# Kernel optimization log

Measured on AMD Instinct MI355X. Metric: run time of the kernel, lower is better.

The kernel has to match this reference:

```python
import jax, jax.numpy as jnp
import numpy as np

LN_EPS = 1e-5


def _conv2d(x, w, b, pad):
    # x: [B,C,H,W], w: [O,I,k,k] (torch OIHW layout)
    out = jax.lax.conv_general_dilated(
        x, w, (1, 1), [(pad, pad), (pad, pad)],
        dimension_numbers=('NCHW', 'OIHW', 'NCHW'))
    return out + b[None, :, None, None]


def _deform_conv2d(x, offset, w, b, k, pad):
    # torchvision.ops.deform_conv2d, offset_groups=1, stride=1, dilation=1.
    # offset layout: [B, 2*k*k, H, W] with (dy, dx) interleaved per kernel tap.
    B, C, H, W = x.shape
    off = offset.reshape(B, k * k, 2, H, W)
    dy, dx = off[:, :, 0], off[:, :, 1]                      # [B,kk,H,W]
    ky, kx = jnp.meshgrid(jnp.arange(k, dtype=x.dtype),
                          jnp.arange(k, dtype=x.dtype), indexing='ij')
    py = (jnp.arange(H, dtype=x.dtype)[None, None, :, None]
          - pad + ky.reshape(-1)[None, :, None, None] + dy)   # sample rows
    px = (jnp.arange(W, dtype=x.dtype)[None, None, None, :]
          - pad + kx.reshape(-1)[None, :, None, None] + dx)   # sample cols
    y0 = jnp.floor(py)
    x0 = jnp.floor(px)
    fy = py - y0
    fx = px - x0
    xf = x.reshape(B, C, H * W)
    gather = jax.vmap(lambda xb, ib: xb[:, ib])               # [C,HW],[K]->[C,K]

    def corner(yc, xc, wt):
        valid = (yc >= 0) & (yc < H) & (xc >= 0) & (xc < W)
        idx = (jnp.clip(yc, 0, H - 1) * W
               + jnp.clip(xc, 0, W - 1)).astype(jnp.int32).reshape(B, -1)
        g = gather(xf, idx).reshape(B, C, k * k, H, W)
        return g * (wt * valid.astype(x.dtype))[:, None]

    # bilinear sample with zero padding outside the image
    acc = (corner(y0, x0, (1 - fy) * (1 - fx))
           + corner(y0, x0 + 1, (1 - fy) * fx)
           + corner(y0 + 1, x0, fy * (1 - fx))
           + corner(y0 + 1, x0 + 1, fy * fx))                 # [B,C,kk,H,W]
    out = jnp.einsum('bckhw,ock->bohw', acc, w.reshape(w.shape[0], C, k * k))
    return out + b[None, :, None, None]


def _deform_branch(xs, off_w, off_b, conv_w, conv_b, k, pad):
    # DeformableConv2d.forward: offset conv, deform_conv2d with conv's own
    # weight/bias, then the plain conv applied AGAIN on the result.
    offset = _conv2d(xs, off_w, off_b, pad)
    d = _deform_conv2d(xs, offset, conv_w, conv_b, k, pad)
    return _conv2d(d, conv_w, conv_b, pad)


def reference(x, H, W, fc1_w, fc1_b, off3_w, off3_b, conv3_w, conv3_b,
              off5_w, off5_b, conv5_w, conv5_b, ln_g, ln_b, fc2_w, fc2_b):
    B, N, _ = x.shape
    h = x @ fc1_w.T + fc1_b                                  # [B,N,hid]
    C = h.shape[-1]
    C2 = C // 2
    x1 = jnp.transpose(h[..., :C2], (0, 2, 1)).reshape(B, C2, H, W)
    x2 = jnp.transpose(h[..., C2:], (0, 2, 1)).reshape(B, C2, H, W)
    x1 = _deform_branch(x1, off3_w, off3_b, conv3_w, conv3_b, 3, 1)
    x2 = _deform_branch(x2, off5_w, off5_b, conv5_w, conv5_b, 5, 2)
    y = jnp.concatenate([x1, x2], axis=1)                    # [B,C,H,W]
    y = jnp.transpose(y.reshape(B, C, N), (0, 2, 1))         # [B,N,C]
    mu = jnp.mean(y, axis=-1, keepdims=True)
    var = jnp.mean(jnp.square(y - mu), axis=-1, keepdims=True)
    y = (y - mu) * jax.lax.rsqrt(var + LN_EPS) * ln_g + ln_b
    y = jax.nn.gelu(y, approximate=False)                    # nn.GELU default
    return y @ fc2_w.T + fc2_b


def setup_inputs() -> dict:
    key = jax.random.key(0)
    ks = jax.random.split(key, 16)
    B, H, W, Cin, Chid = 4, 32, 32, 256, 1024
    C2 = Chid // 2
    N = H * W
    r = lambda k, s, sc: jax.random.normal(k, s, dtype=jnp.float32) * sc
    return {
        'x': r(ks[0], (B, N, Cin), 1.0),
        'H': H, 'W': W,
        'fc1_w': r(ks[1], (Chid, Cin), 0.02),
        'fc1_b': r(ks[2], (Chid,), 0.02),
        'off3_w': r(ks[3], (2 * 9, C2, 3, 3), 0.01),
        'off3_b': r(ks[4], (2 * 9,), 0.01),
        'conv3_w': r(ks[5], (C2, C2, 3, 3), 0.02),
        'conv3_b': r(ks[6], (C2,), 0.02),
        'off5_w': r(ks[7], (2 * 25, C2, 5, 5), 0.01),
        'off5_b': r(ks[8], (2 * 25,), 0.01),
        'conv5_w': r(ks[9], (C2, C2, 5, 5), 0.02),
        'conv5_b': r(ks[10], (C2,), 0.02),
        'ln_g': jnp.ones((Chid,), jnp.float32),
        'ln_b': jnp.zeros((Chid,), jnp.float32),
        'fc2_w': r(ks[11], (Cin, Chid), 0.02),
        'fc2_b': r(ks[12], (Cin,), 0.02),
    }
```

## Files before the change

### kernel.cpp

```cpp
#include <hip/hip_runtime.h>

#define B_    4
#define H_    32
#define W_    32
#define N_    1024
#define CIN_  256
#define CHID_ 1024
#define C2_   512

typedef __attribute__((ext_vector_type(8))) short short8b;
typedef __attribute__((ext_vector_type(4))) float f32x4;

__device__ __forceinline__ unsigned int f2bf2(float lo, float hi) {
    unsigned int ul = __float_as_uint(lo);
    unsigned int uh = __float_as_uint(hi);
    ul += 0x7fffu + ((ul >> 16) & 1u);
    uh += 0x7fffu + ((uh >> 16) & 1u);
    return (ul >> 16) | (uh & 0xffff0000u);
}
__device__ __forceinline__ unsigned short f2bf(float f) {
    unsigned int u = __float_as_uint(f);
    u += 0x7fffu + ((u >> 16) & 1u);
    return (unsigned short)(u >> 16);
}
__device__ __forceinline__ unsigned int cvtpk(float lo, float hi) {
    unsigned int r;
    asm("v_cvt_pk_bf16_f32 %0, %1, %2" : "=v"(r) : "v"(lo), "v"(hi));
    return r;
}
__device__ __forceinline__ float bflo(unsigned int u) { return __uint_as_float(u << 16); }
__device__ __forceinline__ float bfhi(unsigned int u) { return __uint_as_float(u & 0xffff0000u); }

#define ROWP 40
#define MFMA_(a, b, c) __builtin_amdgcn_mfma_f32_16x16x32_bf16(a, b, c, 0, 0, 0)

template<int X> struct Log2 { static constexpr int v = 1 + Log2<X/2>::v; };
template<> struct Log2<1> { static constexpr int v = 0; };

struct ASet { uint4 r0, r1, r2, r3; float4 cw; };
struct BSet { short8b b0, b1, b2, b3; };

template<int AMODE, int KS, int CH, int OUTMODE, int GX, int IMGX = 0>
__global__ __launch_bounds__(512, 2)
void cgemm(const void* __restrict__ Asrc, int lda,
           const unsigned short* __restrict__ Bp, int nk32,
           int tcnt, int KK,
           const float* __restrict__ bias, void* __restrict__ Cout,
           int ldo, int O, int nO16,
           const short4* __restrict__ cidx, const float4* __restrict__ cwt)
{
    constexpr int CHS = Log2<CH>::v;
    __shared__ unsigned short As[2][2][64 * ROWP];

    const int tid = threadIdx.x;
    int m0, o0, tbeg, zslab;
    if constexpr (GX > 0) {
        const int bid = blockIdx.x;
        if constexpr (IMGX) {
            const int b8 = bid & 7, rest = bid >> 3;
            o0 = ((((b8 & 1) << 1) | (rest & 1))) * 128;
            m0 = (((b8 >> 1) << 4) | (rest >> 1)) * 64;
        } else {
            o0 = (bid & (GX - 1)) * 128;
            m0 = (bid / GX) * 64;
        }
        tbeg = 0; zslab = 0;
    } else {
        o0 = 0;
        m0 = blockIdx.y * 64;
        zslab = blockIdx.z;
        tbeg = zslab * tcnt;
    }

    const int srow = tid >> 3;
    const int sk8  = (tid & 7) << 3;
    const int am = m0 + srow;
    const int an = am & (N_ - 1), ab = am >> 10;
    const int ay = an >> 5, ax = an & 31;

    const int lane = tid & 63, wid = tid >> 6;
    const int wr = (wid >> 2) * 32, wc = (wid & 3) * 32;
    const int l15 = lane & 15, lk = (lane >> 4) * 8;

    const int o16a = min((o0 + wc) >> 4, nO16 - 1);
    const int o16b = min((o0 + wc + 16) >> 4, nO16 - 1);
    const unsigned short* bbA = Bp + (size_t)o16a * nk32 * 512 + lane * 8;
    const unsigned short* bbB = Bp + (size_t)o16b * nk32 * 512 + lane * 8;

    const int T = tcnt << CHS;
    const int qbase = (tbeg << CHS) * 2;

    const float* fp = nullptr;
    const unsigned short* sp = nullptr;
    bool svalid = false;
    const unsigned short *g0p = nullptr, *g1p = nullptr,
                         *g2p = nullptr, *g3p = nullptr;
    float4 curCw = {0.f, 0.f, 0.f, 0.f};
    short4 ciPref = {0, 0, 0, 0};
    float4 cwPref = {0.f, 0.f, 0.f, 0.f};

    if constexpr (AMODE == 0) {
        fp = (const float*)Asrc + (size_t)am * lda + sk8;
    } else if constexpr (AMODE == 2) {
        ciPref = cidx[(size_t)am * KK + tbeg];
        cwPref = cwt [(size_t)am * KK + tbeg];
    }

    auto advanceTap = [&](int tp) {
        if constexpr (AMODE == 1) {
            const int PAD = KS / 2;
            const int ty = tp / KS, tx = tp - ty * KS;
            const int yy = ay + ty - PAD, xx = ax + tx - PAD;
            svalid = (yy >= 0 && yy < H_ && xx >= 0 && xx < W_);
            if (svalid)
                sp = (const unsigned short*)Asrc
                   + (size_t)((ab << 10) | (yy << 5) | xx) * lda + sk8;
        } else if constexpr (AMODE == 2) {
            const unsigned short* base = (const unsigned short*)Asrc;
            g0p = base + (size_t)(int)ciPref.x * lda + sk8;
            g1p = base + (size_t)(int)ciPref.y * lda + sk8;
            g2p = base + (size_t)(int)ciPref.z * lda + sk8;
            g3p = base + (size_t)(int)ciPref.w * lda + sk8;
            curCw = cwPref;
            if (tp + 1 < tbeg + tcnt) {
                ciPref = cidx[(size_t)am * KK + tp + 1];
                cwPref = cwt [(size_t)am * KK + tp + 1];
            }
        }
    };

    auto loadRaw = [&](ASet& S, int u) {
        if constexpr (AMODE == 0) {
            S.r0 = *(const uint4*)(fp + (u << 6));
            S.r1 = *(const uint4*)(fp + (u << 6) + 4);
        } else if constexpr (AMODE == 1) {
            S.r0 = svalid ? *(const uint4*)(sp + (u << 6))
                          : make_uint4(0u, 0u, 0u, 0u);
        } else {
            S.r0 = *(const uint4*)(g0p + (u << 6));
            S.r1 = *(const uint4*)(g1p + (u << 6));
            S.r2 = *(const uint4*)(g2p + (u << 6));
            S.r3 = *(const uint4*)(g3p + (u << 6));
            S.cw = curCw;
        }
    };

    auto bl1 = [](unsigned a, unsigned b, unsigned c, unsigned d, float4 cw) {
        const float lo = cw.x * bflo(a) + cw.y * bflo(b)
                       + cw.z * bflo(c) + cw.w * bflo(d);
        const float hi = cw.x * bfhi(a) + cw.y * bfhi(b)
                       + cw.z * bfhi(c) + cw.w * bfhi(d);
        return cvtpk(lo, hi);
    };

    auto blendWrite = [&](ASet& S, int buf) {
        uint4 o;
        if constexpr (AMODE == 0) {
            o = make_uint4(cvtpk(__uint_as_float(S.r0.x), __uint_as_float(S.r0.y)),
                           cvtpk(__uint_as_float(S.r0.z), __uint_as_float(S.r0.w)),
                           cvtpk(__uint_as_float(S.r1.x), __uint_as_float(S.r1.y)),
                           cvtpk(__uint_as_float(S.r1.z), __uint_as_float(S.r1.w)));
        } else if constexpr (AMODE == 1) {
            o = S.r0;
        } else {
            o = make_uint4(bl1(S.r0.x, S.r1.x, S.r2.x, S.r3.x, S.cw),
                           bl1(S.r0.y, S.r1.y, S.r2.y, S.r3.y, S.cw),
                           bl1(S.r0.z, S.r1.z, S.r2.z, S.r3.z, S.cw),
                           bl1(S.r0.w, S.r1.w, S.r2.w, S.r3.w, S.cw));
        }
        *(uint4*)&As[buf][sk8 >> 5][srow * ROWP + (sk8 & 31)] = o;
    };

    auto loadB = [&](BSet& Bv, int g) {
        const int q = qbase + 2 * g;
        Bv.b0 = *(const short8b*)(bbA + (size_t)q * 512);
        Bv.b1 = *(const short8b*)(bbA + (size_t)(q + 1) * 512);
        Bv.b2 = *(const short8b*)(bbB + (size_t)q * 512);
        Bv.b3 = *(const short8b*)(bbB + (size_t)(q + 1) * 512);
    };

    f32x4 acc[2][2];
#pragma unroll
    for (int i = 0; i < 2; ++i)
#pragma unroll
        for (int j = 0; j < 2; ++j)
            acc[i][j] = (f32x4){0.f, 0.f, 0.f, 0.f};

    ASet S0, S1; BSet B0, B1;

    advanceTap(tbeg);
    {
        ASet P;
        loadRaw(P, 0);
        blendWrite(P, 0);
    }
    loadRaw(S0, 1);
    loadB(B0, 0);
    __syncthreads();

    int cur = 0;

    auto iter = [&](int g, ASet& N, ASet& F, BSet& bc, BSet& bn) {
        if (g + 1 < T) loadB(bn, g + 1);
        if (g + 2 < T) {
            const int gn = g + 2;
            if ((gn & (CH - 1)) == 0) advanceTap(tbeg + (gn >> CHS));
            loadRaw(F, gn & (CH - 1));
        }
        if (g + 1 < T) blendWrite(N, cur ^ 1);

        const unsigned short* a0 = As[cur][0];
        const unsigned short* a1 = As[cur][1];
        const short8b af00 = *(const short8b*)(a0 + (wr      + l15) * ROWP + lk);
        const short8b af01 = *(const short8b*)(a0 + (wr + 16 + l15) * ROWP + lk);
        const short8b af10 = *(const short8b*)(a1 + (wr      + l15) * ROWP + lk);
        const short8b af11 = *(const short8b*)(a1 + (wr + 16 + l15) * ROWP + lk);

        acc[0][0] = MFMA_(af00, bc.b0, acc[0][0]);
        acc[0][1] = MFMA_(af00, bc.b2, acc[0][1]);
        acc[1][0] = MFMA_(af01, bc.b0, acc[1][0]);
        acc[1][1] = MFMA_(af01, bc.b2, acc[1][1]);
        acc[0][0] = MFMA_(af10, bc.b1, acc[0][0]);
        acc[0][1] = MFMA_(af10, bc.b3, acc[0][1]);
        acc[1][0] = MFMA_(af11, bc.b1, acc[1][0]);
        acc[1][1] = MFMA_(af11, bc.b3, acc[1][1]);

        __syncthreads();
        cur ^= 1;
    };

    for (int g = 0; g < T; g += 2) {
        iter(g,     S0, S1, B0, B1);
        iter(g + 1, S1, S0, B1, B0);
    }

    const int row0 = m0 + wr + (lane >> 4) * 4;
    const int col0 = o0 + wc + l15;
#pragma unroll
    for (int j = 0; j < 2; ++j) {
        const int cc = col0 + j * 16;
        if (cc < O) {
#pragma unroll
            for (int i = 0; i < 2; ++i)
#pragma unroll
                for (int r = 0; r < 4; ++r) {
                    const int row = row0 + i * 16 + r;
                    if constexpr (OUTMODE == 0)
                        ((float*)Cout)[(size_t)row * ldo + cc] = acc[i][j][r] + bias[cc];
                    else if constexpr (OUTMODE == 1)
                        ((unsigned short*)Cout)[(size_t)row * ldo + cc] =
                            f2bf(acc[i][j][r] + bias[cc]);
                    else
                        ((float*)Cout)[(size_t)zslab * (B_ * N_) * 64
                                       + (size_t)row * 64 + cc] = acc[i][j][r];
                }
        }
    }
}

__global__ void pack_w(const float* __restrict__ w, unsigned short* __restrict__ dst,
                       int Ovalid, int Opad, int obase, int Kc, int KK, int t0, int Ktot)
{
    const int gid = blockIdx.x * blockDim.x + threadIdx.x;
    if (gid >= Opad * Ktot) return;
    const int k  = gid % Ktot;
    const int od = gid / Ktot;
    float v = 0.f;
    if (od < Ovalid) {
        const size_t o = obase + od;
        if (KK == 1) {
            v = w[o * Kc + k];
        } else {
            const int t = t0 + (k >> 9);
            const int c = k & 511;
            v = w[(o * Kc + c) * KK + t];
        }
    }
    const int o16 = od >> 4, l = od & 15, k32 = k >> 5;
    const size_t di = ((size_t)(o16 * (Ktot >> 5) + k32) * 64
                       + (l + ((k >> 3) & 3) * 16)) * 8 + (k & 7);
    dst[di] = f2bf(v);
}

__global__ void pack_conv(const float* __restrict__ w, unsigned short* __restrict__ dst,
                          int O, int KK)
{
    const int gid = blockIdx.x * blockDim.x + threadIdx.x;
    if (gid >= O * 256) return;
    const int c2 = gid & 255;
    const int o  = gid >> 8;
    const int c  = c2 << 1;
    const float* src = w + ((size_t)o * 512 + c) * KK;
    const int nk32 = KK << 4;
    const int o16 = o >> 4, l = o & 15;
    for (int t = 0; t < KK; ++t) {
        const float v0 = src[t];
        const float v1 = src[KK + t];
        const int k = t * 512 + c;
        const size_t di = ((size_t)(o16 * nk32 + (k >> 5)) * 64
                           + (l + ((k >> 3) & 3) * 16)) * 8 + (k & 7);
        *(unsigned int*)&dst[di] = f2bf2(v0, v1);
    }
}

template<int KS, int Z>
__global__ void coeff_kernel(const float* __restrict__ offp,
                             const float* __restrict__ ob,
                             short4* __restrict__ cidx, float4* __restrict__ cwt)
{
    const int KK = KS * KS, PAD = KS / 2;
    const int gid = blockIdx.x * blockDim.x + threadIdx.x;
    if (gid >= B_ * N_ * KK) return;
    const int t = gid % KK;
    const int n = (gid / KK) & (N_ - 1);
    const int b = gid / (KK * N_);
    const int mtok = b * N_ + n;

    const int SL = B_ * N_ * 64;
    float dy = ob[2 * t], dx = ob[2 * t + 1];
#pragma unroll
    for (int z = 0; z < Z; ++z) {
        dy += offp[(size_t)z * SL + (size_t)mtok * 64 + 2 * t];
        dx += offp[(size_t)z * SL + (size_t)mtok * 64 + 2 * t + 1];
    }

    const int y = n >> 5, x = n & 31;
    const float py = (float)(y - PAD + t / KS) + dy;
    const float px = (float)(x - PAD + t % KS) + dx;
    const float y0f = floorf(py), x0f = floorf(px);
    const float fy = py - y0f, fx = px - x0f;
    const int y0 = (int)y0f, x0 = (int)x0f;

    int idx[4]; float wt[4];
    const int   yy[4] = {y0, y0, y0 + 1, y0 + 1};
    const int   xx[4] = {x0, x0 + 1, x0, x0 + 1};
    const float ww[4] = {(1.f - fy) * (1.f - fx), (1.f - fy) * fx,
                         fy * (1.f - fx),         fy * fx};
#pragma unroll
    for (int r = 0; r < 4; ++r) {
        const bool v = (yy[r] >= 0 && yy[r] < H_ && xx[r] >= 0 && xx[r] < W_);
        const int yc = min(max(yy[r], 0), H_ - 1);
        const int xc = min(max(xx[r], 0), W_ - 1);
        idx[r] = b * N_ + yc * W_ + xc;
        wt[r] = v ? ww[r] : 0.f;
    }
    cidx[(size_t)mtok * KK + t] =
        make_short4((short)idx[0], (short)idx[1], (short)idx[2], (short)idx[3]);
    cwt[(size_t)mtok * KK + t] = make_float4(wt[0], wt[1], wt[2], wt[3]);
}

__global__ __launch_bounds__(256)
void ln_gelu(float* __restrict__ ytok, const float* __restrict__ g,
             const float* __restrict__ bt)
{
    const int t = blockIdx.x;
    const int tid = threadIdx.x;
    float* row = ytok + (size_t)t * CHID_;

    float4 v = *(const float4*)&row[tid << 2];
    __shared__ float red[4];

    float s = v.x + v.y + v.z + v.w;
#pragma unroll
    for (int o = 32; o > 0; o >>= 1) s += __shfl_down(s, o, 64);
    if ((tid & 63) == 0) red[tid >> 6] = s;
    __syncthreads();
    const float mean = (red[0] + red[1] + red[2] + red[3]) * (1.f / CHID_);

    const float d0 = v.x - mean, d1 = v.y - mean, d2 = v.z - mean, d3 = v.w - mean;
    float q = d0 * d0 + d1 * d1 + d2 * d2 + d3 * d3;
#pragma unroll
    for (int o = 32; o > 0; o >>= 1) q += __shfl_down(q, o, 64);
    __syncthreads();
    if ((tid & 63) == 0) red[tid >> 6] = q;
    __syncthreads();
    const float var = (red[0] + red[1] + red[2] + red[3]) * (1.f / CHID_);
    const float rstd = rsqrtf(var + 1e-5f);

    const float4 gv = *(const float4*)&g[tid << 2];
    const float4 bv = *(const float4*)&bt[tid << 2];
    float o0 = d0 * rstd * gv.x + bv.x;
    float o1 = d1 * rstd * gv.y + bv.y;
    float o2 = d2 * rstd * gv.z + bv.z;
    float o3 = d3 * rstd * gv.w + bv.w;
    o0 = 0.5f * o0 * (1.f + erff(o0 * 0.70710678118654752f));
    o1 = 0.5f * o1 * (1.f + erff(o1 * 0.70710678118654752f));
    o2 = 0.5f * o2 * (1.f + erff(o2 * 0.70710678118654752f));
    o3 = 0.5f * o3 * (1.f + erff(o3 * 0.70710678118654752f));
    *(float4*)&row[tid << 2] = make_float4(o0, o1, o2, o3);
}

extern "C" void kernel_launch(void* const* d_in, const int* in_sizes, int n_in,
                              void* d_out, int out_size, void* d_ws, size_t ws_size,
                              hipStream_t stream) {
    const float* x       = (const float*)d_in[0];
    const float* fc1_w   = (const float*)d_in[3];
    const float* fc1_b   = (const float*)d_in[4];
    const float* off3_w  = (const float*)d_in[5];
    const float* off3_b  = (const float*)d_in[6];
    const float* conv3_w = (const float*)d_in[7];
    const float* conv3_b = (const float*)d_in[8];
    const float* off5_w  = (const float*)d_in[9];
    const float* off5_b  = (const float*)d_in[10];
    const float* conv5_w = (const float*)d_in[11];
    const float* conv5_b = (const float*)d_in[12];
    const float* ln_g    = (const float*)d_in[13];
    const float* ln_b    = (const float*)d_in[14];
    const float* fc2_w   = (const float*)d_in[15];
    const float* fc2_b   = (const float*)d_in[16];
    float* out = (float*)d_out;

    char* ws = (char*)d_ws;
    float*          ytok   = (float*)(ws);
    float*          offp   = (float*)(ws);
    short4*         cidx3  = (short4*)(ws + 5242880);
    float4*         cwt3   = (float4*)(ws + 5537792);
    short4*         cidx5  = (short4*)(ws + 16777216);
    float4*         cwt5   = (float4*)(ws + 17596416);
    unsigned short* hb     = (unsigned short*)(ws + 19234816);
    unsigned short* fc1wb  = (unsigned short*)(ws + 27623424);
    unsigned short* off3wb = (unsigned short*)(ws + 28147712);
    unsigned short* off5wb = (unsigned short*)(ws + 28737536);
    unsigned short* daccb  = (unsigned short*)(ws + 27623424);
    unsigned short* fc2wb  = (unsigned short*)(ws + 31817728);
    unsigned short* conv3wb= (unsigned short*)(ws + 32342016);
    unsigned short* conv5wb= (unsigned short*)(ws + 37060608);

    const dim3 TB(256);
    const dim3 TG(512);

    pack_w<<<(1024*256 + 255)/256, TB, 0, stream>>>(fc1_w, fc1wb, 1024, 1024, 0, 256, 1, 0, 256);
    pack_w<<<(256*1024 + 255)/256, TB, 0, stream>>>(fc2_w, fc2wb, 256, 256, 0, 1024, 1, 0, 1024);
    pack_w<<<(64*4608  + 255)/256, TB, 0, stream>>>(off3_w, off3wb, 18, 64, 0, 512, 9, 0, 4608);
    pack_w<<<(64*12800 + 255)/256, TB, 0, stream>>>(off5_w, off5wb, 50, 64, 0, 512, 25, 0, 12800);
    pack_conv<<<(512*256 + 255)/256, TB, 0, stream>>>(conv3_w, conv3wb, 512, 9);
    pack_conv<<<(512*256 + 255)/256, TB, 0, stream>>>(conv5_w, conv5wb, 512, 25);

    cgemm<0,1,4,1,8><<<8*64, TG, 0, stream>>>(
        x, CIN_, fc1wb, 8, 1, 1, fc1_b, hb, CHID_, CHID_, 64, nullptr, nullptr);

    cgemm<1,3,8,2,0><<<dim3(1,64,3), TG, 0, stream>>>(
        hb, CHID_, off3wb, 144, 3, 1, nullptr, offp, 64, 18, 4, nullptr, nullptr);
    coeff_kernel<3,3><<<(B_*N_*9 + 255)/256, TB, 0, stream>>>(offp, off3_b, cidx3, cwt3);
    cgemm<1,5,8,2,0><<<dim3(1,64,5), TG, 0, stream>>>(
        hb + C2_, CHID_, off5wb, 400, 5, 1, nullptr, offp, 64, 50, 4, nullptr, nullptr);
    coeff_kernel<5,5><<<(B_*N_*25 + 255)/256, TB, 0, stream>>>(offp, off5_b, cidx5, cwt5);

    cgemm<2,3,8,1,4,1><<<4*64, TG, 0, stream>>>(
        hb, CHID_, conv3wb, 144, 9, 9, conv3_b, daccb, C2_, C2_, 32, cidx3, cwt3);
    cgemm<1,3,8,0,4,1><<<4*64, TG, 0, stream>>>(
        daccb, C2_, conv3wb, 144, 9, 1, conv3_b, ytok, CHID_, C2_, 32, nullptr, nullptr);

    cgemm<2,5,8,1,4,1><<<4*64, TG, 0, stream>>>(
        hb + C2_, CHID_, conv5wb, 400, 25, 25, conv5_b, daccb, C2_, C2_, 32, cidx5, cwt5);
    cgemm<1,5,8,0,4,1><<<4*64, TG, 0, stream>>>(
        daccb, C2_, conv5wb, 400, 25, 1, conv5_b, ytok + C2_, CHID_, C2_, 32, nullptr, nullptr);

    ln_gelu<<<B_*N_, TB, 0, stream>>>(ytok, ln_g, ln_b);
    cgemm<0,1,16,0,2><<<2*64, TG, 0, stream>>>(
        ytok, CHID_, fc2wb, 32, 1, 1, fc2_b, out, CIN_, CIN_, 16, nullptr, nullptr);
}
```

Baseline: 676.2 us.

## Shrink GEMM tiles to 16 rows with 256-thread blocks and restructured pipeline

Reworks the shared cgemm kernel from 64x128 tiles with 512 threads to 16x128 tiles with 256 threads. Each wave now owns 32 output columns across all 16 rows. The K loop is restructured into tap-by-pair iterations with a two-group register prefetch, and grids are made four times larger. The aim is more blocks and higher occupancy for the small-M problem. The cost is less reuse of each B-fragment load, which is fetched per 16 rows instead of per 32, and so more global weight traffic.

```diff
diff --git a/kernel.cpp b/kernel.cpp
--- a/kernel.cpp
+++ b/kernel.cpp
@@ -30,18 +30,21 @@
 }
 __device__ __forceinline__ float bflo(unsigned int u) { return __uint_as_float(u << 16); }
 __device__ __forceinline__ float bfhi(unsigned int u) { return __uint_as_float(u & 0xffff0000u); }
+__device__ __forceinline__ float uf(unsigned int u) { return __uint_as_float(u); }
 
 #define ROWP 40
 #define MFMA_(a, b, c) __builtin_amdgcn_mfma_f32_16x16x32_bf16(a, b, c, 0, 0, 0)
 
-template<int X> struct Log2 { static constexpr int v = 1 + Log2<X/2>::v; };
-template<> struct Log2<1> { static constexpr int v = 0; };
-
-struct ASet { uint4 r0, r1, r2, r3; float4 cw; };
-struct BSet { short8b b0, b1, b2, b3; };
+struct Grp {
+    uint2 a0, a1, b0, b1, c0, c1, d0, d1;
+    uint4 q0, q1;
+    uint2 p0, p1;
+    float4 cw;
+};
+struct BB { short8b f000, f001, f010, f011, f100, f101, f110, f111; };
 
 template<int AMODE, int KS, int CH, int OUTMODE, int GX, int IMGX = 0>
-__global__ __launch_bounds__(512, 2)
+__global__ __launch_bounds__(256, 4)
 void cgemm(const void* __restrict__ Asrc, int lda,
            const unsigned short* __restrict__ Bp, int nk32,
            int tcnt, int KK,
@@ -49,8 +52,8 @@
            int ldo, int O, int nO16,
            const short4* __restrict__ cidx, const float4* __restrict__ cwt)
 {
-    constexpr int CHS = Log2<CH>::v;
-    __shared__ unsigned short As[2][2][64 * ROWP];
+    constexpr int PP = CH / 2;
+    __shared__ unsigned short As[2][2][2][16 * ROWP];
 
     const int tid = threadIdx.x;
     int m0, o0, tbeg, zslab;
@@ -58,37 +61,33 @@
         const int bid = blockIdx.x;
         if constexpr (IMGX) {
             const int b8 = bid & 7, rest = bid >> 3;
-            o0 = ((((b8 & 1) << 1) | (rest & 1))) * 128;
-            m0 = (((b8 >> 1) << 4) | (rest >> 1)) * 64;
+            o0 = (((b8 & 1) << 1) | (rest & 1)) * 128;
+            m0 = (b8 >> 1) * 1024 + (rest >> 1) * 16;
         } else {
             o0 = (bid & (GX - 1)) * 128;
-            m0 = (bid / GX) * 64;
+            m0 = (bid / GX) * 16;
         }
         tbeg = 0; zslab = 0;
     } else {
-        o0 = 0;
-        m0 = blockIdx.y * 64;
-        zslab = blockIdx.z;
-        tbeg = zslab * tcnt;
-    }
-
-    const int srow = tid >> 3;
-    const int sk8  = (tid & 7) << 3;
+        o0 = 0; m0 = blockIdx.y * 16;
+        zslab = blockIdx.z; tbeg = zslab * tcnt;
+    }
+    const int tend = tbeg + tcnt;
+
+    const int srow = tid >> 4;
+    const int sk4  = (tid & 15) << 2;
     const int am = m0 + srow;
     const int an = am & (N_ - 1), ab = am >> 10;
     const int ay = an >> 5, ax = an & 31;
 
     const int lane = tid & 63, wid = tid >> 6;
-    const int wr = (wid >> 2) * 32, wc = (wid & 3) * 32;
     const int l15 = lane & 15, lk = (lane >> 4) * 8;
-
-    const int o16a = min((o0 + wc) >> 4, nO16 - 1);
-    const int o16b = min((o0 + wc + 16) >> 4, nO16 - 1);
-    const unsigned short* bbA = Bp + (size_t)o16a * nk32 * 512 + lane * 8;
-    const unsigned short* bbB = Bp + (size_t)o16b * nk32 * 512 + lane * 8;
-
-    const int T = tcnt << CHS;
-    const int qbase = (tbeg << CHS) * 2;
+    const int o16a = min((o0 + wid * 32) >> 4, nO16 - 1);
+    const int o16b = min((o0 + wid * 32 + 16) >> 4, nO16 - 1);
+    const unsigned short* bb0 =
+        Bp + ((size_t)o16a * nk32 + tbeg * 2 * CH) * 512 + lane * 8;
+    const unsigned short* bb1 =
+        Bp + ((size_t)o16b * nk32 + tbeg * 2 * CH) * 512 + lane * 8;
 
     const float* fp = nullptr;
     const unsigned short* sp = nullptr;
@@ -100,7 +99,7 @@
     float4 cwPref = {0.f, 0.f, 0.f, 0.f};
 
     if constexpr (AMODE == 0) {
-        fp = (const float*)Asrc + (size_t)am * lda + sk8;
+        fp = (const float*)Asrc + (size_t)am * lda + sk4;
     } else if constexpr (AMODE == 2) {
         ciPref = cidx[(size_t)am * KK + tbeg];
         cwPref = cwt [(size_t)am * KK + tbeg];
@@ -114,34 +113,33 @@
             svalid = (yy >= 0 && yy < H_ && xx >= 0 && xx < W_);
             if (svalid)
                 sp = (const unsigned short*)Asrc
-                   + (size_t)((ab << 10) | (yy << 5) | xx) * lda + sk8;
+                   + (size_t)((ab << 10) | (yy << 5) | xx) * lda + sk4;
         } else if constexpr (AMODE == 2) {
             const unsigned short* base = (const unsigned short*)Asrc;
-            g0p = base + (size_t)(int)ciPref.x * lda + sk8;
-            g1p = base + (size_t)(int)ciPref.y * lda + sk8;
-            g2p = base + (size_t)(int)ciPref.z * lda + sk8;
-            g3p = base + (size_t)(int)ciPref.w * lda + sk8;
+            g0p = base + (size_t)(int)ciPref.x * lda + sk4;
+            g1p = base + (size_t)(int)ciPref.y * lda + sk4;
+            g2p = base + (size_t)(int)ciPref.z * lda + sk4;
+            g3p = base + (size_t)(int)ciPref.w * lda + sk4;
             curCw = cwPref;
-            if (tp + 1 < tbeg + tcnt) {
-                ciPref = cidx[(size_t)am * KK + tp + 1];
-                cwPref = cwt [(size_t)am * KK + tp + 1];
-            }
-        }
-    };
-
-    auto loadRaw = [&](ASet& S, int u) {
+            const int tnx = min(tp + 1, tend - 1);
+            ciPref = cidx[(size_t)am * KK + tnx];
+            cwPref = cwt [(size_t)am * KK + tnx];
+        }
+    };
+
+    auto issuePair = [&](Grp& g, int s0, int s1) {
         if constexpr (AMODE == 0) {
-            S.r0 = *(const uint4*)(fp + (u << 6));
-            S.r1 = *(const uint4*)(fp + (u << 6) + 4);
+            g.q0 = *(const uint4*)(fp + s0 * 64);
+            g.q1 = *(const uint4*)(fp + s1 * 64);
         } else if constexpr (AMODE == 1) {
-            S.r0 = svalid ? *(const uint4*)(sp + (u << 6))
-                          : make_uint4(0u, 0u, 0u, 0u);
+            g.p0 = svalid ? *(const uint2*)(sp + s0 * 64) : make_uint2(0u, 0u);
+            g.p1 = svalid ? *(const uint2*)(sp + s1 * 64) : make_uint2(0u, 0u);
         } else {
-            S.r0 = *(const uint4*)(g0p + (u << 6));
-            S.r1 = *(const uint4*)(g1p + (u << 6));
-            S.r2 = *(const uint4*)(g2p + (u << 6));
-            S.r3 = *(const uint4*)(g3p + (u << 6));
-            S.cw = curCw;
+            g.a0 = *(const uint2*)(g0p + s0 * 64); g.a1 = *(const uint2*)(g0p + s1 * 64);
+            g.b0 = *(const uint2*)(g1p + s0 * 64); g.b1 = *(const uint2*)(g1p + s1 * 64);
+            g.c0 = *(const uint2*)(g2p + s0 * 64); g.c1 = *(const uint2*)(g2p + s1 * 64);
+            g.d0 = *(const uint2*)(g3p + s0 * 64); g.d1 = *(const uint2*)(g3p + s1 * 64);
+            g.cw = curCw;
         }
     };
 
@@ -153,107 +151,113 @@
         return cvtpk(lo, hi);
     };
 
-    auto blendWrite = [&](ASet& S, int buf) {
-        uint4 o;
+    auto blendPair = [&](Grp& g, int par) {
+        unsigned short* d0 = &As[par][0][sk4 >> 5][srow * ROWP + (sk4 & 31)];
+        unsigned short* d1 = &As[par][1][sk4 >> 5][srow * ROWP + (sk4 & 31)];
         if constexpr (AMODE == 0) {
-            o = make_uint4(cvtpk(__uint_as_float(S.r0.x), __uint_as_float(S.r0.y)),
-                           cvtpk(__uint_as_float(S.r0.z), __uint_as_float(S.r0.w)),
-                           cvtpk(__uint_as_float(S.r1.x), __uint_as_float(S.r1.y)),
-                           cvtpk(__uint_as_float(S.r1.z), __uint_as_float(S.r1.w)));
+            *(uint2*)d0 = make_uint2(cvtpk(uf(g.q0.x), uf(g.q0.y)),
+                                     cvtpk(uf(g.q0.z), uf(g.q0.w)));
+            *(uint2*)d1 = make_uint2(cvtpk(uf(g.q1.x), uf(g.q1.y)),
+                                     cvtpk(uf(g.q1.z), uf(g.q1.w)));
         } else if constexpr (AMODE == 1) {
-            o = S.r0;
+            *(uint2*)d0 = g.p0;
+            *(uint2*)d1 = g.p1;
         } else {
-            o = make_uint4(bl1(S.r0.x, S.r1.x, S.r2.x, S.r3.x, S.cw),
-                           bl1(S.r0.y, S.r1.y, S.r2.y, S.r3.y, S.cw),
-                           bl1(S.r0.z, S.r1.z, S.r2.z, S.r3.z, S.cw),
-                           bl1(S.r0.w, S.r1.w, S.r2.w, S.r3.w, S.cw));
-        }
-        *(uint4*)&As[buf][sk8 >> 5][srow * ROWP + (sk8 & 31)] = o;
-    };
-
-    auto loadB = [&](BSet& Bv, int g) {
-        const int q = qbase + 2 * g;
-        Bv.b0 = *(const short8b*)(bbA + (size_t)q * 512);
-        Bv.b1 = *(const short8b*)(bbA + (size_t)(q + 1) * 512);
-        Bv.b2 = *(const short8b*)(bbB + (size_t)q * 512);
-        Bv.b3 = *(const short8b*)(bbB + (size_t)(q + 1) * 512);
-    };
-
-    f32x4 acc[2][2];
-#pragma unroll
-    for (int i = 0; i < 2; ++i)
-#pragma unroll
-        for (int j = 0; j < 2; ++j)
-            acc[i][j] = (f32x4){0.f, 0.f, 0.f, 0.f};
-
-    ASet S0, S1; BSet B0, B1;
-
-    advanceTap(tbeg);
-    {
-        ASet P;
-        loadRaw(P, 0);
-        blendWrite(P, 0);
-    }
-    loadRaw(S0, 1);
-    loadB(B0, 0);
+            *(uint2*)d0 = make_uint2(bl1(g.a0.x, g.b0.x, g.c0.x, g.d0.x, g.cw),
+                                     bl1(g.a0.y, g.b0.y, g.c0.y, g.d0.y, g.cw));
+            *(uint2*)d1 = make_uint2(bl1(g.a1.x, g.b1.x, g.c1.x, g.d1.x, g.cw),
+                                     bl1(g.a1.y, g.b1.y, g.c1.y, g.d1.y, g.cw));
+        }
+    };
+
+    BB Bc;
+    auto loadB = [&]() {
+        Bc.f000 = *(const short8b*)(bb0);
+        Bc.f001 = *(const short8b*)(bb0 + 512);
+        Bc.f010 = *(const short8b*)(bb0 + 1024);
+        Bc.f011 = *(const short8b*)(bb0 + 1536);
+        Bc.f100 = *(const short8b*)(bb1);
+        Bc.f101 = *(const short8b*)(bb1 + 512);
+        Bc.f110 = *(const short8b*)(bb1 + 1024);
+        Bc.f111 = *(const short8b*)(bb1 + 1536);
+    };
+    auto bumpB = [&]() { bb0 += 2048; bb1 += 2048; };
+
+    f32x4 acc[2];
+    acc[0] = (f32x4){0.f, 0.f, 0.f, 0.f};
+    acc[1] = (f32x4){0.f, 0.f, 0.f, 0.f};
+
+    auto mfmaPair = [&](int par) {
+        const short8b a00 = *(const short8b*)&As[par][0][0][l15 * ROWP + lk];
+        const short8b a01 = *(const short8b*)&As[par][0][1][l15 * ROWP + lk];
+        const short8b a10 = *(const short8b*)&As[par][1][0][l15 * ROWP + lk];
+        const short8b a11 = *(const short8b*)&As[par][1][1][l15 * ROWP + lk];
+        acc[0] = MFMA_(a00, Bc.f000, acc[0]);  acc[1] = MFMA_(a00, Bc.f100, acc[1]);
+        acc[0] = MFMA_(a01, Bc.f001, acc[0]);  acc[1] = MFMA_(a01, Bc.f101, acc[1]);
+        acc[0] = MFMA_(a10, Bc.f010, acc[0]);  acc[1] = MFMA_(a10, Bc.f110, acc[1]);
+        acc[0] = MFMA_(a11, Bc.f011, acc[0]);  acc[1] = MFMA_(a11, Bc.f111, acc[1]);
+    };
+
+    Grp G0, G1;
+
+    if constexpr (AMODE != 0) advanceTap(tbeg);
+    issuePair(G0, 0, 1);
+    blendPair(G0, 0);
+    issuePair(G1, 2, 3);
     __syncthreads();
 
-    int cur = 0;
-
-    auto iter = [&](int g, ASet& N, ASet& F, BSet& bc, BSet& bn) {
-        if (g + 1 < T) loadB(bn, g + 1);
-        if (g + 2 < T) {
-            const int gn = g + 2;
-            if ((gn & (CH - 1)) == 0) advanceTap(tbeg + (gn >> CHS));
-            loadRaw(F, gn & (CH - 1));
-        }
-        if (g + 1 < T) blendWrite(N, cur ^ 1);
-
-        const unsigned short* a0 = As[cur][0];
-        const unsigned short* a1 = As[cur][1];
-        const short8b af00 = *(const short8b*)(a0 + (wr      + l15) * ROWP + lk);
-        const short8b af01 = *(const short8b*)(a0 + (wr + 16 + l15) * ROWP + lk);
-        const short8b af10 = *(const short8b*)(a1 + (wr      + l15) * ROWP + lk);
-        const short8b af11 = *(const short8b*)(a1 + (wr + 16 + l15) * ROWP + lk);
-
-        acc[0][0] = MFMA_(af00, bc.b0, acc[0][0]);
-        acc[0][1] = MFMA_(af00, bc.b2, acc[0][1]);
-        acc[1][0] = MFMA_(af01, bc.b0, acc[1][0]);
-        acc[1][1] = MFMA_(af01, bc.b2, acc[1][1]);
-        acc[0][0] = MFMA_(af10, bc.b1, acc[0][0]);
-        acc[0][1] = MFMA_(af10, bc.b3, acc[0][1]);
-        acc[1][0] = MFMA_(af11, bc.b1, acc[1][0]);
-        acc[1][1] = MFMA_(af11, bc.b3, acc[1][1]);
-
+    for (int t = tbeg; t < tend - 1; ++t) {
+#pragma unroll
+        for (int p = 0; p < PP; ++p) {
+            loadB();
+            if (p == PP - 2) advanceTap(t + 1);
+            {
+                const int s0 = ((p + 2) % PP) * 2;
+                if ((p & 1) == 0) issuePair(G0, s0, s0 + 1);
+                else              issuePair(G1, s0, s0 + 1);
+            }
+            if ((p & 1) == 0) blendPair(G1, 1);
+            else              blendPair(G0, 0);
+            mfmaPair(p & 1);
+            __syncthreads();
+            bumpB();
+        }
+    }
+#pragma unroll
+    for (int p = 0; p < PP; ++p) {
+        loadB();
+        if (p < PP - 2) {
+            const int s0 = (p + 2) * 2;
+            if ((p & 1) == 0) issuePair(G0, s0, s0 + 1);
+            else              issuePair(G1, s0, s0 + 1);
+        }
+        if (p <= PP - 2) {
+            if ((p & 1) == 0) blendPair(G1, 1);
+            else              blendPair(G0, 0);
+        }
+        mfmaPair(p & 1);
         __syncthreads();
-        cur ^= 1;
-    };
-
-    for (int g = 0; g < T; g += 2) {
-        iter(g,     S0, S1, B0, B1);
-        iter(g + 1, S1, S0, B1, B0);
-    }
-
-    const int row0 = m0 + wr + (lane >> 4) * 4;
-    const int col0 = o0 + wc + l15;
+        bumpB();
+    }
+
+    const int row0 = m0 + (lane >> 4) * 4;
+    const int colb = o0 + wid * 32 + l15;
 #pragma unroll
     for (int j = 0; j < 2; ++j) {
-        const int cc = col0 + j * 16;
+        const int cc = colb + j * 16;
         if (cc < O) {
 #pragma unroll
-            for (int i = 0; i < 2; ++i)
-#pragma unroll
-                for (int r = 0; r < 4; ++r) {
-                    const int row = row0 + i * 16 + r;
-                    if constexpr (OUTMODE == 0)
-                        ((float*)Cout)[(size_t)row * ldo + cc] = acc[i][j][r] + bias[cc];
-                    else if constexpr (OUTMODE == 1)
-                        ((unsigned short*)Cout)[(size_t)row * ldo + cc] =
-                            f2bf(acc[i][j][r] + bias[cc]);
-                    else
-                        ((float*)Cout)[(size_t)zslab * (B_ * N_) * 64
-                                       + (size_t)row * 64 + cc] = acc[i][j][r];
-                }
+            for (int r = 0; r < 4; ++r) {
+                const int row = row0 + r;
+                if constexpr (OUTMODE == 0)
+                    ((float*)Cout)[(size_t)row * ldo + cc] = acc[j][r] + bias[cc];
+                else if constexpr (OUTMODE == 1)
+                    ((unsigned short*)Cout)[(size_t)row * ldo + cc] =
+                        f2bf(acc[j][r] + bias[cc]);
+                else
+                    ((float*)Cout)[(size_t)zslab * (B_ * N_) * 64
+                                   + (size_t)row * 64 + cc] = acc[j][r];
+            }
         }
     }
 }
@@ -427,7 +431,6 @@
     unsigned short* conv5wb= (unsigned short*)(ws + 37060608);
 
     const dim3 TB(256);
-    const dim3 TG(512);
 
     pack_w<<<(1024*256 + 255)/256, TB, 0, stream>>>(fc1_w, fc1wb, 1024, 1024, 0, 256, 1, 0, 256);
     pack_w<<<(256*1024 + 255)/256, TB, 0, stream>>>(fc2_w, fc2wb, 256, 256, 0, 1024, 1, 0, 1024);
@@ -436,27 +439,27 @@
     pack_conv<<<(512*256 + 255)/256, TB, 0, stream>>>(conv3_w, conv3wb, 512, 9);
     pack_conv<<<(512*256 + 255)/256, TB, 0, stream>>>(conv5_w, conv5wb, 512, 25);
 
-    cgemm<0,1,4,1,8><<<8*64, TG, 0, stream>>>(
+    cgemm<0,1,4,1,8><<<8*256, TB, 0, stream>>>(
         x, CIN_, fc1wb, 8, 1, 1, fc1_b, hb, CHID_, CHID_, 64, nullptr, nullptr);
 
-    cgemm<1,3,8,2,0><<<dim3(1,64,3), TG, 0, stream>>>(
+    cgemm<1,3,8,2,0><<<dim3(1,256,3), TB, 0, stream>>>(
         hb, CHID_, off3wb, 144, 3, 1, nullptr, offp, 64, 18, 4, nullptr, nullptr);
     coeff_kernel<3,3><<<(B_*N_*9 + 255)/256, TB, 0, stream>>>(offp, off3_b, cidx3, cwt3);
-    cgemm<1,5,8,2,0><<<dim3(1,64,5), TG, 0, stream>>>(
+    cgemm<1,5,8,2,0><<<dim3(1,256,5), TB, 0, stream>>>(
         hb + C2_, CHID_, off5wb, 400, 5, 1, nullptr, offp, 64, 50, 4, nullptr, nullptr);
     coeff_kernel<5,5><<<(B_*N_*25 + 255)/256, TB, 0, stream>>>(offp, off5_b, cidx5, cwt5);
 
-    cgemm<2,3,8,1,4,1><<<4*64, TG, 0, stream>>>(
+    cgemm<2,3,8,1,4,1><<<1024, TB, 0, stream>>>(
         hb, CHID_, conv3wb, 144, 9, 9, conv3_b, daccb, C2_, C2_, 32, cidx3, cwt3);
-    cgemm<1,3,8,0,4,1><<<4*64, TG, 0, stream>>>(
+    cgemm<1,3,8,0,4,1><<<1024, TB, 0, stream>>>(
         daccb, C2_, conv3wb, 144, 9, 1, conv3_b, ytok, CHID_, C2_, 32, nullptr, nullptr);
 
-    cgemm<2,5,8,1,4,1><<<4*64, TG, 0, stream>>>(
+    cgemm<2,5,8,1,4,1><<<1024, TB, 0, stream>>>(
         hb + C2_, CHID_, conv5wb, 400, 25, 25, conv5_b, daccb, C2_, C2_, 32, cidx5, cwt5);
-    cgemm<1,5,8,0,4,1><<<4*64, TG, 0, stream>>>(
+    cgemm<1,5,8,0,4,1><<<1024, TB, 0, stream>>>(
         daccb, C2_, conv5wb, 400, 25, 1, conv5_b, ytok + C2_, CHID_, C2_, 32, nullptr, nullptr);
 
     ln_gelu<<<B_*N_, TB, 0, stream>>>(ytok, ln_g, ln_b);
-    cgemm<0,1,16,0,2><<<2*64, TG, 0, stream>>>(
+    cgemm<0,1,16,0,2><<<2*256, TB, 0, stream>>>(
         ytok, CHID_, fc2wb, 32, 1, 1, fc2_b, out, CIN_, CIN_, 16, nullptr, nullptr);
 }
```

After: 688.4 us. About the same (+1.8%).
